# Kernel optimization log

Measured on AMD Instinct MI355X. Metric: run time of the kernel, lower is better.

The kernel has to match this reference:

```python
import jax, jax.numpy as jnp
import numpy as np

N_ELEM = 5
N_ROWS = 16            # height slices contained in the minibatch
N = 512                # sample_size_n
MB = N_ROWS * N        # minibatch_size = 8192
NVOX = MB * N          # n_voxel_minibatch
N_LINES = 12
LINE_GROUPS = [3, 2, 3, 2, 2]
SAMPLE_SIZE_CM = np.float32(0.01)
PROBE_CTS = np.float32(1.0e5)
FL_RATIO = np.float32(0.0017)   # fl_sig_collecting_ratio
SA_ADJ = np.float32(1.0)        # solid_angle_adjustment_factor
SA_THETA = np.float32(1.0)      # selfAb == False -> SA_theta = 1


def _rotate(arr, theta):
    # torch affine_grid + grid_sample(bilinear, padding_mode='border', align_corners=False)
    # arr: (E, C, H, W); rotation matrix rows [cos, -sin, 0], [sin, cos, 0]
    E, C, H, W = arr.shape
    cos, sin = jnp.cos(theta), jnp.sin(theta)
    xs = (2.0 * jnp.arange(W, dtype=arr.dtype) + 1.0) / W - 1.0
    ys = (2.0 * jnp.arange(H, dtype=arr.dtype) + 1.0) / H - 1.0
    gy, gx = jnp.meshgrid(ys, xs, indexing='ij')      # (H, W)
    x_in = cos * gx - sin * gy
    y_in = sin * gx + cos * gy
    ix = jnp.clip(((x_in + 1.0) * W - 1.0) * 0.5, 0.0, W - 1.0)  # border padding
    iy = jnp.clip(((y_in + 1.0) * H - 1.0) * 0.5, 0.0, H - 1.0)
    x0 = jnp.floor(ix); y0 = jnp.floor(iy)
    wx = ix - x0; wy = iy - y0
    x0i = x0.astype(jnp.int32); y0i = y0.astype(jnp.int32)
    x1i = jnp.minimum(x0i + 1, W - 1); y1i = jnp.minimum(y0i + 1, H - 1)
    g = lambda yi, xi: arr[:, :, yi, xi]              # -> (E, C, H, W)
    return (g(y0i, x0i) * (1 - wx) * (1 - wy) + g(y0i, x1i) * wx * (1 - wy)
            + g(y1i, x0i) * (1 - wx) * wy + g(y1i, x1i) * wx * wy)


def setup_inputs() -> dict:
    key = jax.random.key(0)
    k1, k2, k3 = jax.random.split(key, 3)
    xp = jax.random.uniform(k1, (N_ELEM, N_ROWS, N, N), dtype=jnp.float32)
    probe_attCS_ls = jax.random.uniform(k2, (N_ELEM,), dtype=jnp.float32) * 10.0
    detected_fl_unit_concentration = jax.random.uniform(k3, (N_LINES,), dtype=jnp.float32)
    line_element_idx = jnp.asarray(np.repeat(np.arange(N_ELEM), LINE_GROUPS).astype(np.int32))
    theta = jnp.float32(np.pi / 6)
    return {"xp": xp, "probe_attCS_ls": probe_attCS_ls,
            "detected_fl_unit_concentration": detected_fl_unit_concentration,
            "theta": theta, "line_element_idx": line_element_idx}


def reference(xp, probe_attCS_ls, detected_fl_unit_concentration, theta, line_element_idx):
    # rotate concentration grid and flatten beam rows: (E, MB, N)
    conc = _rotate(xp, theta).reshape(N_ELEM, MB, N)
    # Beer-Lambert attenuation: per-element lac summed over elements, cumsum along beam
    lac = jnp.einsum('e,ebs->bs', probe_attCS_ls, conc)                       # (MB, N)
    att_acc = jnp.pad(jnp.cumsum(lac, axis=1) * (SAMPLE_SIZE_CM / N),
                      ((0, 0), (1, 0)))                                       # (MB, N+1)
    attenuation_flat = jnp.exp(-att_acc[:, :-1]).reshape(NVOX)
    transmission = att_acc[:, -1]                                             # (MB,)
    # fluorescence map: each line picks its element's concentration
    conc_flat = conc.reshape(N_ELEM, NVOX)
    fl_map = conc_flat[line_element_idx] * detected_fl_unit_concentration[:, None]  # (L, NVOX)
    probe_after = PROBE_CTS * attenuation_flat
    fl_sig = (probe_after[None, :] * fl_map * SA_THETA).reshape(N_LINES, MB, N).sum(axis=-1)
    fl_sig = fl_sig * FL_RATIO * SA_ADJ                                       # (L, MB)
    return fl_sig, transmission
```

## Files before the change

kernel.cpp:

```cpp
#include <hip/hip_runtime.h>
#include <hip/hip_bf16.h>

#define MB_ROWS  8192
#define N_LINES  12
#define SCALE    (0.01f / 512.0f)
#define FL_CONST 170.0f

struct __attribute__((packed, aligned(4))) F2 { float x, y; };

__global__ __launch_bounds__(512) void fused_fl_kernel(
    const float* __restrict__ xp,
    const float* __restrict__ attCS,
    const float* __restrict__ dfl,
    const float* __restrict__ theta_p,
    const int*   __restrict__ lidx,
    float*       __restrict__ out)
{
    const int bid = blockIdx.x;
    const int t   = bid >> 3;
    const int c   = (bid & 7) + 8 * (t >> 6);
    const int g   = t & 63;
    const int irow0 = g << 3;

    const int tid  = threadIdx.x;
    const int r    = tid & 7;
    const int sc   = tid >> 3;
    const int lane = tid & 63;
    const int w    = tid >> 6;

    const float theta = theta_p[0];
    const float cs = cosf(theta);
    const float sn = sinf(theta);

    const float gyr = (2.0f * (float)(irow0 + r) + 1.0f) * (1.0f / 512.0f) - 1.0f;

    const size_t estride = (size_t)16 * 512 * 512;
    const float* base = xp + (size_t)c * (512 * 512);

    const float a0 = attCS[0], a1 = attCS[1], a2 = attCS[2], a3 = attCS[3], a4 = attCS[4];

    __shared__ float s_x[2][6][8][72];

    float se0 = 0.f, se1 = 0.f, se2 = 0.f, se3 = 0.f, se4 = 0.f;
    float carry = 0.f;

    for (int k = 0; k < 8; ++k) {
        const int buf = k & 1;

        {
            const int s = sc + (k << 6);
            const float gx = (2.0f * (float)s + 1.0f) * (1.0f / 512.0f) - 1.0f;
            const float x_in = cs * gx - sn * gyr;
            const float y_in = sn * gx + cs * gyr;
            float ix = ((x_in + 1.0f) * 512.0f - 1.0f) * 0.5f;
            float iy = ((y_in + 1.0f) * 512.0f - 1.0f) * 0.5f;
            ix = fminf(fmaxf(ix, 0.0f), 511.0f);
            iy = fminf(fmaxf(iy, 0.0f), 511.0f);

            const float x0f = floorf(ix);
            const float y0f = floorf(iy);
            const float wx = ix - x0f;
            const float wy = iy - y0f;
            const int x0 = (int)x0f;
            const int y0 = (int)y0f;
            const int y1 = min(y0 + 1, 511);

            const bool edge = (x0 >= 511);
            const int  xL   = edge ? 510 : x0;

            const float w1y0 = wx * (1.0f - wy);
            const float w1y1 = wx * wy;
            const float w0y0 = (1.0f - wx) * (1.0f - wy);
            const float w0y1 = (1.0f - wx) * wy;

            const int oA = y0 * 512 + xL;
            const int oB = y1 * 512 + xL;

            float cv[5];
            const float* p = base;
#pragma unroll
            for (int e = 0; e < 5; ++e) {
                const F2 pa = *(const F2*)(p + oA);
                const F2 pb = *(const F2*)(p + oB);
                const float vA0 = edge ? pa.y : pa.x;
                const float vB0 = edge ? pb.y : pb.x;
                float acc = w0y0 * vA0;
                acc = fmaf(w1y0, pa.y, acc);
                acc = fmaf(w0y1, vB0, acc);
                acc = fmaf(w1y1, pb.y, acc);
                cv[e] = acc;
                p += estride;
            }

            float lac = a0 * cv[0];
            lac = fmaf(a1, cv[1], lac);
            lac = fmaf(a2, cv[2], lac);
            lac = fmaf(a3, cv[3], lac);
            lac = fmaf(a4, cv[4], lac);

            s_x[buf][0][r][sc] = cv[0];
            s_x[buf][1][r][sc] = cv[1];
            s_x[buf][2][r][sc] = cv[2];
            s_x[buf][3][r][sc] = cv[3];
            s_x[buf][4][r][sc] = cv[4];
            s_x[buf][5][r][sc] = lac;
        }

        __syncthreads();

        {
            const float lv = s_x[buf][5][w][lane];
            float v = lv;
#pragma unroll
            for (int off = 1; off < 64; off <<= 1) {
                float n = __shfl_up(v, off, 64);
                if (lane >= off) v += n;
            }
            const float tot  = __shfl(v, 63, 64);
            const float excl = carry + v - lv;
            const float att  = __expf(-excl * SCALE);
            carry += tot;

            const float d0 = s_x[buf][0][w][lane];
            const float d1 = s_x[buf][1][w][lane];
            const float d2 = s_x[buf][2][w][lane];
            const float d3 = s_x[buf][3][w][lane];
            const float d4 = s_x[buf][4][w][lane];
            se0 = fmaf(att, d0, se0);
            se1 = fmaf(att, d1, se1);
            se2 = fmaf(att, d2, se2);
            se3 = fmaf(att, d3, se3);
            se4 = fmaf(att, d4, se4);
        }
    }

#pragma unroll
    for (int off = 32; off > 0; off >>= 1) {
        se0 += __shfl_down(se0, off, 64);
        se1 += __shfl_down(se1, off, 64);
        se2 += __shfl_down(se2, off, 64);
        se3 += __shfl_down(se3, off, 64);
        se4 += __shfl_down(se4, off, 64);
    }
    const float S0 = __shfl(se0, 0, 64);
    const float S1 = __shfl(se1, 0, 64);
    const float S2 = __shfl(se2, 0, 64);
    const float S3 = __shfl(se3, 0, 64);
    const float S4 = __shfl(se4, 0, 64);

    const size_t b = (size_t)c * 512 + irow0 + w;
    if (lane == 0) {
        out[(size_t)N_LINES * MB_ROWS + b] = carry * SCALE;
    }
    if (lane < N_LINES) {
        const int li = lidx[lane];
        float Ssel = S0;
        Ssel = (li == 1) ? S1 : Ssel;
        Ssel = (li == 2) ? S2 : Ssel;
        Ssel = (li == 3) ? S3 : Ssel;
        Ssel = (li == 4) ? S4 : Ssel;
        out[(size_t)lane * MB_ROWS + b] = FL_CONST * dfl[lane] * Ssel;
    }
}

extern "C" void kernel_launch(void* const* d_in, const int* in_sizes, int n_in,
                              void* d_out, int out_size, void* d_ws, size_t ws_size,
                              hipStream_t stream) {
    const float* xp    = (const float*)d_in[0];
    const float* attCS = (const float*)d_in[1];
    const float* dfl   = (const float*)d_in[2];
    const float* theta = (const float*)d_in[3];
    const int*   lidx  = (const int*)d_in[4];
    float* out = (float*)d_out;

    fused_fl_kernel<<<MB_ROWS / 8, 512, 0, stream>>>(xp, attCS, dfl, theta, lidx, out);
}
```

Before: 171.2 us.

## Split into LDS-tiled rotate kernel with fp16 workspace plus row-scan kernel

```diff
diff --git a/kernel.cpp b/kernel.cpp
--- a/kernel.cpp
+++ b/kernel.cpp
@@ -5,6 +5,205 @@
 #define N_LINES  12
 #define SCALE    (0.01f / 512.0f)
 #define FL_CONST 170.0f
+#define EPLANE   (MB_ROWS * 512)
+#define WS_NEED  (5ull * (unsigned long long)EPLANE * 2ull)
+
+typedef _Float16 half_t;
+
+__global__ __launch_bounds__(256) void rotate_kernel(
+    const float* __restrict__ xp,
+    const float* __restrict__ theta_p,
+    half_t*      __restrict__ conc16)
+{
+    const int bid = blockIdx.x;
+    const int tx = bid & 15;
+    const int ty = (bid >> 4) & 15;
+    const int c  = bid >> 8;
+    const int s0   = tx << 5;
+    const int row0 = ty << 5;
+    const int tid  = threadIdx.x;
+
+    const float theta = theta_p[0];
+    const float cs = cosf(theta);
+    const float sn = sinf(theta);
+
+    const float gxa = (2.0f * (float)s0          + 1.0f) * (1.0f / 512.0f) - 1.0f;
+    const float gxb = (2.0f * (float)(s0 + 31)   + 1.0f) * (1.0f / 512.0f) - 1.0f;
+    const float gya = (2.0f * (float)row0        + 1.0f) * (1.0f / 512.0f) - 1.0f;
+    const float gyb = (2.0f * (float)(row0 + 31) + 1.0f) * (1.0f / 512.0f) - 1.0f;
+
+    const float xi00 = cs * gxa - sn * gya, xi01 = cs * gxa - sn * gyb;
+    const float xi10 = cs * gxb - sn * gya, xi11 = cs * gxb - sn * gyb;
+    const float yi00 = sn * gxa + cs * gya, yi01 = sn * gxa + cs * gyb;
+    const float yi10 = sn * gxb + cs * gya, yi11 = sn * gxb + cs * gyb;
+
+    const float xmn = fminf(fminf(xi00, xi01), fminf(xi10, xi11));
+    const float xmx = fmaxf(fmaxf(xi00, xi01), fmaxf(xi10, xi11));
+    const float ymn = fminf(fminf(yi00, yi01), fminf(yi10, yi11));
+    const float ymx = fmaxf(fmaxf(yi00, yi01), fmaxf(yi10, yi11));
+
+    const float ixmn = fminf(fmaxf(((xmn + 1.0f) * 512.0f - 1.0f) * 0.5f, 0.0f), 511.0f);
+    const float ixmx = fminf(fmaxf(((xmx + 1.0f) * 512.0f - 1.0f) * 0.5f, 0.0f), 511.0f);
+    const float iymn = fminf(fmaxf(((ymn + 1.0f) * 512.0f - 1.0f) * 0.5f, 0.0f), 511.0f);
+    const float iymx = fminf(fmaxf(((ymx + 1.0f) * 512.0f - 1.0f) * 0.5f, 0.0f), 511.0f);
+
+    const int bbx0 = (int)floorf(ixmn);
+    const int bbx1 = min((int)floorf(ixmx) + 2, 511);
+    const int bby0 = (int)floorf(iymn);
+    const int bby1 = min((int)floorf(iymx) + 2, 511);
+    int W = bbx1 - bbx0 + 1;
+    int H = bby1 - bby0 + 1;
+    if (W > 49) W = 49;
+    if (H > 48) H = 48;
+
+    const size_t estride = (size_t)16 * 512 * 512;
+    const float* base = xp + (size_t)c * (512 * 512);
+
+    __shared__ float tiles[5][48 * 49];
+
+    const int span = H << 6;
+#pragma unroll
+    for (int e = 0; e < 5; ++e) {
+        const float* plane = base + (size_t)e * estride;
+        for (int idx = tid; idx < span; idx += 256) {
+            const int yy = idx >> 6;
+            const int xx = idx & 63;
+            if (xx < W) tiles[e][yy * 49 + xx] = plane[(bby0 + yy) * 512 + bbx0 + xx];
+        }
+    }
+    __syncthreads();
+
+    const int sx = tid & 31;
+    const int ry = tid >> 5;
+    const int s  = s0 + sx;
+    const float gx = (2.0f * (float)s + 1.0f) * (1.0f / 512.0f) - 1.0f;
+
+#pragma unroll
+    for (int q = 0; q < 4; ++q) {
+        const int row = row0 + ry + (q << 3);
+        const float gy = (2.0f * (float)row + 1.0f) * (1.0f / 512.0f) - 1.0f;
+
+        const float x_in = cs * gx - sn * gy;
+        const float y_in = sn * gx + cs * gy;
+        float ix = ((x_in + 1.0f) * 512.0f - 1.0f) * 0.5f;
+        float iy = ((y_in + 1.0f) * 512.0f - 1.0f) * 0.5f;
+        ix = fminf(fmaxf(ix, 0.0f), 511.0f);
+        iy = fminf(fmaxf(iy, 0.0f), 511.0f);
+
+        const float x0f = floorf(ix);
+        const float y0f = floorf(iy);
+        const float wx = ix - x0f;
+        const float wy = iy - y0f;
+        const int x0 = (int)x0f;
+        const int y0 = (int)y0f;
+        const int x1 = min(x0 + 1, 511);
+        const int y1 = min(y0 + 1, 511);
+
+        const float w00 = (1.0f - wx) * (1.0f - wy);
+        const float w01 = wx * (1.0f - wy);
+        const float w10 = (1.0f - wx) * wy;
+        const float w11 = wx * wy;
+
+        const int o00 = (y0 - bby0) * 49 + (x0 - bbx0);
+        const int o01 = (y0 - bby0) * 49 + (x1 - bbx0);
+        const int o10 = (y1 - bby0) * 49 + (x0 - bbx0);
+        const int o11 = (y1 - bby0) * 49 + (x1 - bbx0);
+
+        const size_t ob = (size_t)(c * 512 + row) * 512 + s;
+#pragma unroll
+        for (int e = 0; e < 5; ++e) {
+            const float* tp = tiles[e];
+            const float v = w00 * tp[o00] + w01 * tp[o01]
+                          + w10 * tp[o10] + w11 * tp[o11];
+            conc16[(size_t)e * EPLANE + ob] = (half_t)v;
+        }
+    }
+}
+
+__global__ __launch_bounds__(512) void scan_fl_kernel(
+    const half_t* __restrict__ conc16,
+    const float*  __restrict__ attCS,
+    const float*  __restrict__ dfl,
+    const int*    __restrict__ lidx,
+    float*        __restrict__ out)
+{
+    const int tid  = threadIdx.x;
+    const int lane = tid & 63;
+    const int w    = tid >> 6;
+    const int b    = blockIdx.x * 8 + w;
+
+    union Ld { uint4 u; half_t h[8]; };
+    Ld ld[5];
+#pragma unroll
+    for (int e = 0; e < 5; ++e) {
+        ld[e].u = *(const uint4*)(conc16 + (size_t)e * EPLANE + (size_t)b * 512 + lane * 8);
+    }
+
+    const float a[5] = { attCS[0], attCS[1], attCS[2], attCS[3], attCS[4] };
+
+    float p[8];
+    float run = 0.0f;
+#pragma unroll
+    for (int j = 0; j < 8; ++j) {
+        float lac = a[0] * (float)ld[0].h[j];
+        lac = fmaf(a[1], (float)ld[1].h[j], lac);
+        lac = fmaf(a[2], (float)ld[2].h[j], lac);
+        lac = fmaf(a[3], (float)ld[3].h[j], lac);
+        lac = fmaf(a[4], (float)ld[4].h[j], lac);
+        run += lac;
+        p[j] = run;
+    }
+
+    float v = run;
+#pragma unroll
+    for (int off = 1; off < 64; off <<= 1) {
+        float n = __shfl_up(v, off, 64);
+        if (lane >= off) v += n;
+    }
+    const float lane_excl = v - run;
+    const float row_tot   = __shfl(v, 63, 64);
+
+    float se0 = 0.f, se1 = 0.f, se2 = 0.f, se3 = 0.f, se4 = 0.f;
+#pragma unroll
+    for (int j = 0; j < 8; ++j) {
+        const float excl = lane_excl + p[j] - (a[0] * (float)ld[0].h[j]
+                         + a[1] * (float)ld[1].h[j] + a[2] * (float)ld[2].h[j]
+                         + a[3] * (float)ld[3].h[j] + a[4] * (float)ld[4].h[j]);
+        const float att = __expf(-excl * SCALE);
+        se0 = fmaf(att, (float)ld[0].h[j], se0);
+        se1 = fmaf(att, (float)ld[1].h[j], se1);
+        se2 = fmaf(att, (float)ld[2].h[j], se2);
+        se3 = fmaf(att, (float)ld[3].h[j], se3);
+        se4 = fmaf(att, (float)ld[4].h[j], se4);
+    }
+
+#pragma unroll
+    for (int off = 32; off > 0; off >>= 1) {
+        se0 += __shfl_down(se0, off, 64);
+        se1 += __shfl_down(se1, off, 64);
+        se2 += __shfl_down(se2, off, 64);
+        se3 += __shfl_down(se3, off, 64);
+        se4 += __shfl_down(se4, off, 64);
+    }
+    const float S0 = __shfl(se0, 0, 64);
+    const float S1 = __shfl(se1, 0, 64);
+    const float S2 = __shfl(se2, 0, 64);
+    const float S3 = __shfl(se3, 0, 64);
+    const float S4 = __shfl(se4, 0, 64);
+
+    if (lane == 0) {
+        out[(size_t)N_LINES * MB_ROWS + b] = row_tot * SCALE;
+    }
+    if (lane < N_LINES) {
+        const int li = lidx[lane];
+        float Ssel = S0;
+        Ssel = (li == 1) ? S1 : Ssel;
+        Ssel = (li == 2) ? S2 : Ssel;
+        Ssel = (li == 3) ? S3 : Ssel;
+        Ssel = (li == 4) ? S4 : Ssel;
+        out[(size_t)lane * MB_ROWS + b] = FL_CONST * dfl[lane] * Ssel;
+    }
+}
 
 struct __attribute__((packed, aligned(4))) F2 { float x, y; };
 
@@ -46,7 +245,6 @@
 
     for (int k = 0; k < 8; ++k) {
         const int buf = k & 1;
-
         {
             const int s = sc + (k << 6);
             const float gx = (2.0f * (float)s + 1.0f) * (1.0f / 512.0f) - 1.0f;
@@ -121,16 +319,11 @@
             const float att  = __expf(-excl * SCALE);
             carry += tot;
 
-            const float d0 = s_x[buf][0][w][lane];
-            const float d1 = s_x[buf][1][w][lane];
-            const float d2 = s_x[buf][2][w][lane];
-            const float d3 = s_x[buf][3][w][lane];
-            const float d4 = s_x[buf][4][w][lane];
-            se0 = fmaf(att, d0, se0);
-            se1 = fmaf(att, d1, se1);
-            se2 = fmaf(att, d2, se2);
-            se3 = fmaf(att, d3, se3);
-            se4 = fmaf(att, d4, se4);
+            se0 = fmaf(att, s_x[buf][0][w][lane], se0);
+            se1 = fmaf(att, s_x[buf][1][w][lane], se1);
+            se2 = fmaf(att, s_x[buf][2][w][lane], se2);
+            se3 = fmaf(att, s_x[buf][3][w][lane], se3);
+            se4 = fmaf(att, s_x[buf][4][w][lane], se4);
         }
     }
 
@@ -173,5 +366,11 @@
     const int*   lidx  = (const int*)d_in[4];
     float* out = (float*)d_out;
 
-    fused_fl_kernel<<<MB_ROWS / 8, 512, 0, stream>>>(xp, attCS, dfl, theta, lidx, out);
+    if (ws_size >= WS_NEED) {
+        half_t* conc16 = (half_t*)d_ws;
+        rotate_kernel<<<4096, 256, 0, stream>>>(xp, theta, conc16);
+        scan_fl_kernel<<<MB_ROWS / 8, 512, 0, stream>>>(conc16, attCS, dfl, lidx, out);
+    } else {
+        fused_fl_kernel<<<MB_ROWS / 8, 512, 0, stream>>>(xp, attCS, dfl, theta, lidx, out);
+    }
 }
```

Result: slower. 276.5 us (+61.5%).

## Split beam rows into per-wave segments and combine scans via factorized exponentials

Applied to the files above, without the earlier changes.

```diff
diff --git a/kernel.cpp b/kernel.cpp
--- a/kernel.cpp
+++ b/kernel.cpp
@@ -8,7 +8,7 @@
 
 struct __attribute__((packed, aligned(4))) F2 { float x, y; };
 
-__global__ __launch_bounds__(512) void fused_fl_kernel(
+__global__ __launch_bounds__(512, 4) void fused_fl_kernel(
     const float* __restrict__ xp,
     const float* __restrict__ attCS,
     const float* __restrict__ dfl,
@@ -23,10 +23,10 @@
     const int irow0 = g << 3;
 
     const int tid  = threadIdx.x;
-    const int r    = tid & 7;
-    const int sc   = tid >> 3;
     const int lane = tid & 63;
     const int w    = tid >> 6;
+    const int j    = lane & 7;
+    const int r    = lane >> 3;
 
     const float theta = theta_p[0];
     const float cs = cosf(theta);
@@ -39,127 +39,159 @@
 
     const float a0 = attCS[0], a1 = attCS[1], a2 = attCS[2], a3 = attCS[3], a4 = attCS[4];
 
-    __shared__ float s_x[2][6][8][72];
+    __shared__ float s_seg[8][8][6];
 
     float se0 = 0.f, se1 = 0.f, se2 = 0.f, se3 = 0.f, se4 = 0.f;
     float carry = 0.f;
 
     for (int k = 0; k < 8; ++k) {
-        const int buf = k & 1;
-
+        const int s = (w << 6) + (k << 3) + j;
+        const float gx = (2.0f * (float)s + 1.0f) * (1.0f / 512.0f) - 1.0f;
+        const float x_in = cs * gx - sn * gyr;
+        const float y_in = sn * gx + cs * gyr;
+        float ix = ((x_in + 1.0f) * 512.0f - 1.0f) * 0.5f;
+        float iy = ((y_in + 1.0f) * 512.0f - 1.0f) * 0.5f;
+        ix = fminf(fmaxf(ix, 0.0f), 511.0f);
+        iy = fminf(fmaxf(iy, 0.0f), 511.0f);
+
+        const float x0f = floorf(ix);
+        const float y0f = floorf(iy);
+        const float wx = ix - x0f;
+        const float wy = iy - y0f;
+        const int x0 = (int)x0f;
+        const int y0 = (int)y0f;
+        const int y1 = min(y0 + 1, 511);
+
+        const bool edge = (x0 >= 511);
+        const int  xL   = edge ? 510 : x0;
+
+        const float w0y0 = (1.0f - wx) * (1.0f - wy);
+        const float w1y0 = wx * (1.0f - wy);
+        const float w0y1 = (1.0f - wx) * wy;
+        const float w1y1 = wx * wy;
+
+        const int oA = y0 * 512 + xL;
+        const int oB = y1 * 512 + xL;
+
+        float cv0, cv1, cv2, cv3, cv4;
         {
-            const int s = sc + (k << 6);
-            const float gx = (2.0f * (float)s + 1.0f) * (1.0f / 512.0f) - 1.0f;
-            const float x_in = cs * gx - sn * gyr;
-            const float y_in = sn * gx + cs * gyr;
-            float ix = ((x_in + 1.0f) * 512.0f - 1.0f) * 0.5f;
-            float iy = ((y_in + 1.0f) * 512.0f - 1.0f) * 0.5f;
-            ix = fminf(fmaxf(ix, 0.0f), 511.0f);
-            iy = fminf(fmaxf(iy, 0.0f), 511.0f);
-
-            const float x0f = floorf(ix);
-            const float y0f = floorf(iy);
-            const float wx = ix - x0f;
-            const float wy = iy - y0f;
-            const int x0 = (int)x0f;
-            const int y0 = (int)y0f;
-            const int y1 = min(y0 + 1, 511);
-
-            const bool edge = (x0 >= 511);
-            const int  xL   = edge ? 510 : x0;
-
-            const float w1y0 = wx * (1.0f - wy);
-            const float w1y1 = wx * wy;
-            const float w0y0 = (1.0f - wx) * (1.0f - wy);
-            const float w0y1 = (1.0f - wx) * wy;
-
-            const int oA = y0 * 512 + xL;
-            const int oB = y1 * 512 + xL;
-
-            float cv[5];
             const float* p = base;
-#pragma unroll
-            for (int e = 0; e < 5; ++e) {
-                const F2 pa = *(const F2*)(p + oA);
-                const F2 pb = *(const F2*)(p + oB);
-                const float vA0 = edge ? pa.y : pa.x;
-                const float vB0 = edge ? pb.y : pb.x;
-                float acc = w0y0 * vA0;
-                acc = fmaf(w1y0, pa.y, acc);
-                acc = fmaf(w0y1, vB0, acc);
-                acc = fmaf(w1y1, pb.y, acc);
-                cv[e] = acc;
-                p += estride;
-            }
-
-            float lac = a0 * cv[0];
-            lac = fmaf(a1, cv[1], lac);
-            lac = fmaf(a2, cv[2], lac);
-            lac = fmaf(a3, cv[3], lac);
-            lac = fmaf(a4, cv[4], lac);
-
-            s_x[buf][0][r][sc] = cv[0];
-            s_x[buf][1][r][sc] = cv[1];
-            s_x[buf][2][r][sc] = cv[2];
-            s_x[buf][3][r][sc] = cv[3];
-            s_x[buf][4][r][sc] = cv[4];
-            s_x[buf][5][r][sc] = lac;
-        }
-
-        __syncthreads();
-
+            F2 pa, pb;
+            pa = *(const F2*)(p + oA); pb = *(const F2*)(p + oB);
+            cv0 = w0y0 * (edge ? pa.y : pa.x) + w1y0 * pa.y
+                + w0y1 * (edge ? pb.y : pb.x) + w1y1 * pb.y;
+            p += estride;
+            pa = *(const F2*)(p + oA); pb = *(const F2*)(p + oB);
+            cv1 = w0y0 * (edge ? pa.y : pa.x) + w1y0 * pa.y
+                + w0y1 * (edge ? pb.y : pb.x) + w1y1 * pb.y;
+            p += estride;
+            pa = *(const F2*)(p + oA); pb = *(const F2*)(p + oB);
+            cv2 = w0y0 * (edge ? pa.y : pa.x) + w1y0 * pa.y
+                + w0y1 * (edge ? pb.y : pb.x) + w1y1 * pb.y;
+            p += estride;
+            pa = *(const F2*)(p + oA); pb = *(const F2*)(p + oB);
+            cv3 = w0y0 * (edge ? pa.y : pa.x) + w1y0 * pa.y
+                + w0y1 * (edge ? pb.y : pb.x) + w1y1 * pb.y;
+            p += estride;
+            pa = *(const F2*)(p + oA); pb = *(const F2*)(p + oB);
+            cv4 = w0y0 * (edge ? pa.y : pa.x) + w1y0 * pa.y
+                + w0y1 * (edge ? pb.y : pb.x) + w1y1 * pb.y;
+        }
+
+        float lac = a0 * cv0;
+        lac = fmaf(a1, cv1, lac);
+        lac = fmaf(a2, cv2, lac);
+        lac = fmaf(a3, cv3, lac);
+        lac = fmaf(a4, cv4, lac);
+
+        float v = lac;
+#pragma unroll
+        for (int off = 1; off < 8; off <<= 1) {
+            float n = __shfl_up(v, off, 64);
+            if (j >= off) v += n;
+        }
+        const float tot = __shfl(v, lane | 7, 64);
+        const float att = __expf(-(carry + v - lac) * SCALE);
+        carry += tot;
+
+        se0 = fmaf(att, cv0, se0);
+        se1 = fmaf(att, cv1, se1);
+        se2 = fmaf(att, cv2, se2);
+        se3 = fmaf(att, cv3, se3);
+        se4 = fmaf(att, cv4, se4);
+    }
+
+#pragma unroll
+    for (int off = 1; off < 8; off <<= 1) {
+        se0 += __shfl_xor(se0, off, 64);
+        se1 += __shfl_xor(se1, off, 64);
+        se2 += __shfl_xor(se2, off, 64);
+        se3 += __shfl_xor(se3, off, 64);
+        se4 += __shfl_xor(se4, off, 64);
+    }
+
+    if (j == 0) {
+        s_seg[w][r][0] = carry;
+        s_seg[w][r][1] = se0;
+        s_seg[w][r][2] = se1;
+        s_seg[w][r][3] = se2;
+        s_seg[w][r][4] = se3;
+        s_seg[w][r][5] = se4;
+    }
+    __syncthreads();
+
+    if (w == 0) {
+        const int seg = j;
+        const float A = s_seg[seg][r][0];
+
+        float v = A;
+#pragma unroll
+        for (int off = 1; off < 8; off <<= 1) {
+            float n = __shfl_up(v, off, 64);
+            if (seg >= off) v += n;
+        }
+        const float f = __expf(-(v - A) * SCALE);
+
+        float S0 = f * s_seg[seg][r][1];
+        float S1 = f * s_seg[seg][r][2];
+        float S2 = f * s_seg[seg][r][3];
+        float S3 = f * s_seg[seg][r][4];
+        float S4 = f * s_seg[seg][r][5];
+#pragma unroll
+        for (int off = 1; off < 8; off <<= 1) {
+            S0 += __shfl_xor(S0, off, 64);
+            S1 += __shfl_xor(S1, off, 64);
+            S2 += __shfl_xor(S2, off, 64);
+            S3 += __shfl_xor(S3, off, 64);
+            S4 += __shfl_xor(S4, off, 64);
+        }
+
+        const float rowtot = __shfl(v, lane | 7, 64);
+        const size_t b = (size_t)c * 512 + irow0 + r;
+
+        if (seg == 7) {
+            out[(size_t)N_LINES * MB_ROWS + b] = rowtot * SCALE;
+        }
         {
-            const float lv = s_x[buf][5][w][lane];
-            float v = lv;
-#pragma unroll
-            for (int off = 1; off < 64; off <<= 1) {
-                float n = __shfl_up(v, off, 64);
-                if (lane >= off) v += n;
-            }
-            const float tot  = __shfl(v, 63, 64);
-            const float excl = carry + v - lv;
-            const float att  = __expf(-excl * SCALE);
-            carry += tot;
-
-            const float d0 = s_x[buf][0][w][lane];
-            const float d1 = s_x[buf][1][w][lane];
-            const float d2 = s_x[buf][2][w][lane];
-            const float d3 = s_x[buf][3][w][lane];
-            const float d4 = s_x[buf][4][w][lane];
-            se0 = fmaf(att, d0, se0);
-            se1 = fmaf(att, d1, se1);
-            se2 = fmaf(att, d2, se2);
-            se3 = fmaf(att, d3, se3);
-            se4 = fmaf(att, d4, se4);
-        }
-    }
-
-#pragma unroll
-    for (int off = 32; off > 0; off >>= 1) {
-        se0 += __shfl_down(se0, off, 64);
-        se1 += __shfl_down(se1, off, 64);
-        se2 += __shfl_down(se2, off, 64);
-        se3 += __shfl_down(se3, off, 64);
-        se4 += __shfl_down(se4, off, 64);
-    }
-    const float S0 = __shfl(se0, 0, 64);
-    const float S1 = __shfl(se1, 0, 64);
-    const float S2 = __shfl(se2, 0, 64);
-    const float S3 = __shfl(se3, 0, 64);
-    const float S4 = __shfl(se4, 0, 64);
-
-    const size_t b = (size_t)c * 512 + irow0 + w;
-    if (lane == 0) {
-        out[(size_t)N_LINES * MB_ROWS + b] = carry * SCALE;
-    }
-    if (lane < N_LINES) {
-        const int li = lidx[lane];
-        float Ssel = S0;
-        Ssel = (li == 1) ? S1 : Ssel;
-        Ssel = (li == 2) ? S2 : Ssel;
-        Ssel = (li == 3) ? S3 : Ssel;
-        Ssel = (li == 4) ? S4 : Ssel;
-        out[(size_t)lane * MB_ROWS + b] = FL_CONST * dfl[lane] * Ssel;
+            const int l = seg;
+            const int li = lidx[l];
+            float Ssel = S0;
+            Ssel = (li == 1) ? S1 : Ssel;
+            Ssel = (li == 2) ? S2 : Ssel;
+            Ssel = (li == 3) ? S3 : Ssel;
+            Ssel = (li == 4) ? S4 : Ssel;
+            out[(size_t)l * MB_ROWS + b] = FL_CONST * dfl[l] * Ssel;
+        }
+        if (seg < 4) {
+            const int l = seg + 8;
+            const int li = lidx[l];
+            float Ssel = S0;
+            Ssel = (li == 1) ? S1 : Ssel;
+            Ssel = (li == 2) ? S2 : Ssel;
+            Ssel = (li == 3) ? S3 : Ssel;
+            Ssel = (li == 4) ? S4 : Ssel;
+            out[(size_t)l * MB_ROWS + b] = FL_CONST * dfl[l] * Ssel;
+        }
     }
 }
 
```

Result: faster. 159.0 us (-7.1%).
